# Kernel optimization log

Measured on AMD Instinct MI355X. Metric: run time of the kernel, lower is better.

## Reference

```python
import jax, jax.numpy as jnp
import numpy as np

BS = 16
CIN = 32          # input_channels
COUT = 64         # out_channels
OUT_DIM = 1024    # out_dim
S = 2
S0 = 1
K = S * (S0 + 1)  # non-overlapping patch size = 4
D = OUT_DIM * K   # input spatial length = 4096


def setup_inputs() -> dict:
    key = jax.random.key(0)
    k1, k2 = jax.random.split(key)
    x = jax.random.normal(k1, (BS, CIN, D), dtype=jnp.float32)
    # learned parameter, torch.randn init
    weight = jax.random.normal(k2, (COUT, CIN, D), dtype=jnp.float32)
    return {"x": x, "weight": weight}


def reference(x, weight):
    # sharing == 0 path of NonOverlappingLocallyConnected1d:
    #   out[b,o,p] = (1/sqrt(CIN)) * sum_{c,k} x[b,c,p*K+k] * weight[o,c,p*K+k]
    # Original materializes [bs,cout,cin,D] via broadcast multiply then sums
    # over (cin, K); fused here as a single einsum over non-overlapping patches.
    bs = x.shape[0]
    xr = x.reshape(bs, CIN, OUT_DIM, K)        # [b, c, p, k]
    wr = weight.reshape(COUT, CIN, OUT_DIM, K)  # [o, c, p, k]
    out = jnp.einsum('bcpk,ocpk->bop', xr, wr)  # [b, o, p]
    return out / jnp.sqrt(jnp.asarray(CIN, x.dtype))
```

## Files before the change

### kernel.cpp

```cpp
#include <hip/hip_runtime.h>

#define CIN     32
#define COUT    64
#define OUT_DIM 1024
#define RS4     1024

__global__ __launch_bounds__(512, 2) void nolc1d_kernel(
    const float* __restrict__ x,
    const float* __restrict__ w,
    float* __restrict__ out)
{
    const int bid = blockIdx.x;
    const int xcd = bid & 7;
    const int m   = bid >> 3;
    const int og  = m & 3;
    const int pc  = xcd * 8 + (m >> 2);
    const int o0  = og * 16;
    const int pf0 = pc * 16;

    const int t    = threadIdx.x;
    const int lane = t & 63;
    const int wv   = t >> 6;
    const int p    = t & 15;
    const int cs   = (t >> 4) & 1;
    const int g    = (t >> 5) & 3;
    const int oq   = t >> 7;

    __shared__ float4 wls[3][1024];
    __shared__ float4 xls[3][1024];

    const float4* __restrict__ x4 = (const float4*)x;
    const float4* __restrict__ w4 = (const float4*)w;

    const int r4 = lane >> 4;
    const int q  = lane & 15;

    auto stage = [&](int buf, int ci) {
        #pragma unroll
        for (int i = 0; i < 2; ++i) {
            const int s = wv * 2 + i;
            const int c = ci * 4 + r4;
            const float4* srcw =
                &w4[((o0 + s) * CIN + c) * RS4 + pf0 + q];
            __builtin_amdgcn_global_load_lds(
                (const __attribute__((address_space(1))) void*)srcw,
                (__attribute__((address_space(3))) void*)&wls[buf][s * 64],
                16, 0, 0);
            const float4* srcx =
                &x4[(s * CIN + c) * RS4 + pf0 + q];
            __builtin_amdgcn_global_load_lds(
                (const __attribute__((address_space(1))) void*)srcx,
                (__attribute__((address_space(3))) void*)&xls[buf][s * 64],
                16, 0, 0);
        }
    };

    float acc[4][4] = {};

    stage(0, 0);
    stage(1, 1);

    #pragma unroll 1
    for (int ci = 0; ci < 8; ++ci) {
        if (ci < 7) asm volatile("s_waitcnt vmcnt(4)" ::: "memory");
        else        asm volatile("s_waitcnt vmcnt(0)" ::: "memory");
        __builtin_amdgcn_s_barrier();
        if (ci < 6) stage((ci + 2) % 3, ci + 2);
        const int buf = ci % 3;
        #pragma unroll
        for (int jj = 0; jj < 2; ++jj) {
            const int cl = cs * 2 + jj;
            float4 xv[4], wq[4];
            #pragma unroll
            for (int bi = 0; bi < 4; ++bi)
                xv[bi] = xls[buf][((g * 4 + bi) * 4 + cl) * 16 + p];
            #pragma unroll
            for (int oi = 0; oi < 4; ++oi)
                wq[oi] = wls[buf][((oq * 4 + oi) * 4 + cl) * 16 + p];
            #pragma unroll
            for (int bi = 0; bi < 4; ++bi)
                #pragma unroll
                for (int oi = 0; oi < 4; ++oi)
                    acc[bi][oi] += xv[bi].x * wq[oi].x + xv[bi].y * wq[oi].y +
                                   xv[bi].z * wq[oi].z + xv[bi].w * wq[oi].w;
        }
    }

    #pragma unroll
    for (int bi = 0; bi < 4; ++bi)
        #pragma unroll
        for (int oi = 0; oi < 4; ++oi)
            acc[bi][oi] += __shfl_xor(acc[bi][oi], 16, 64);

    const float scale = 0.17677669529663687f;
    if (cs == 0) {
        #pragma unroll
        for (int bi = 0; bi < 4; ++bi)
            #pragma unroll
            for (int oi = 0; oi < 4; ++oi)
                out[((size_t)(4 * g + bi) * COUT + o0 + 4 * oq + oi) * OUT_DIM
                    + pf0 + p] = acc[bi][oi] * scale;
    }
}

extern "C" void kernel_launch(void* const* d_in, const int* in_sizes, int n_in,
                              void* d_out, int out_size, void* d_ws, size_t ws_size,
                              hipStream_t stream) {
    const float* x = (const float*)d_in[0];
    const float* w = (const float*)d_in[1];
    float* out = (float*)d_out;

    nolc1d_kernel<<<dim3(256), dim3(512), 0, stream>>>(x, w, out);
}
```

Measured before the change: 85.72 us.

## Warp-specialize producer/consumer waves with LDS flag handshakes and 4-stage buffers

Splits the block into two loader waves (one for weights, one for x) and four compute waves, synchronized through volatile LDS flags and done counters instead of block-wide barriers. Grows the LDS ring from three to four stages and swizzles the x layout with an XOR to reduce bank conflicts. Each compute wave now covers all four channels per chunk, so the cross-lane shuffle reduction is gone. It adds spin-wait polling and relies on vmcnt ordering for LDS-direct loads being visible to other waves, which is fragile. The 128KB LDS per block may also cap occupancy at one block per CU.

```diff
diff --git a/kernel.cpp b/kernel.cpp
--- a/kernel.cpp
+++ b/kernel.cpp
@@ -5,7 +5,7 @@
 #define OUT_DIM 1024
 #define RS4     1024
 
-__global__ __launch_bounds__(512, 2) void nolc1d_kernel(
+__global__ __launch_bounds__(384, 2) void nolc1d_kernel(
     const float* __restrict__ x,
     const float* __restrict__ w,
     float* __restrict__ out)
@@ -21,85 +21,112 @@
     const int t    = threadIdx.x;
     const int lane = t & 63;
     const int wv   = t >> 6;
-    const int p    = t & 15;
-    const int cs   = (t >> 4) & 1;
-    const int g    = (t >> 5) & 3;
-    const int oq   = t >> 7;
 
-    __shared__ float4 wls[3][1024];
-    __shared__ float4 xls[3][1024];
+    __shared__ float4 wls[4][1024];
+    __shared__ float4 xls[4][1024];
+    __shared__ int flag_w[8];
+    __shared__ int flag_x[8];
+    __shared__ int done[8];
+
+    if (t < 8) { flag_w[t] = 0; flag_x[t] = 0; done[t] = 0; }
+    __syncthreads();
+
+    volatile int* vfw = flag_w;
+    volatile int* vfx = flag_x;
+    volatile int* vdn = done;
 
     const float4* __restrict__ x4 = (const float4*)x;
     const float4* __restrict__ w4 = (const float4*)w;
 
-    const int r4 = lane >> 4;
-    const int q  = lane & 15;
+    if (wv == 0) {
+        const int cl = lane >> 4;
+        const int q  = lane & 15;
+        #pragma unroll 1
+        for (int ci = 0; ci < 8; ++ci) {
+            if (ci >= 4) while (vdn[ci - 4] < 4) __builtin_amdgcn_s_sleep(1);
+            const int buf = ci & 3;
+            #pragma unroll
+            for (int s = 0; s < 16; ++s) {
+                const float4* src =
+                    &w4[((o0 + s) * CIN + ci * 4 + cl) * RS4 + pf0 + q];
+                __builtin_amdgcn_global_load_lds(
+                    (const __attribute__((address_space(1))) void*)src,
+                    (__attribute__((address_space(3))) void*)&wls[buf][s * 64],
+                    16, 0, 0);
+            }
+            if (ci >= 2) {
+                asm volatile("s_waitcnt vmcnt(32)" ::: "memory");
+                vfw[ci - 2] = 1;
+            }
+        }
+        asm volatile("s_waitcnt vmcnt(16)" ::: "memory");
+        vfw[6] = 1;
+        asm volatile("s_waitcnt vmcnt(0)" ::: "memory");
+        vfw[7] = 1;
+    } else if (wv == 1) {
+        const int cl = lane >> 4;
+        #pragma unroll 1
+        for (int ci = 0; ci < 8; ++ci) {
+            if (ci >= 4) while (vdn[ci - 4] < 4) __builtin_amdgcn_s_sleep(1);
+            const int buf = ci & 3;
+            #pragma unroll
+            for (int s = 0; s < 16; ++s) {
+                const int qs = (lane & 15) ^ (s >> 2);
+                const float4* src =
+                    &x4[(s * CIN + ci * 4 + cl) * RS4 + pf0 + qs];
+                __builtin_amdgcn_global_load_lds(
+                    (const __attribute__((address_space(1))) void*)src,
+                    (__attribute__((address_space(3))) void*)&xls[buf][s * 64],
+                    16, 0, 0);
+            }
+            if (ci >= 2) {
+                asm volatile("s_waitcnt vmcnt(32)" ::: "memory");
+                vfx[ci - 2] = 1;
+            }
+        }
+        asm volatile("s_waitcnt vmcnt(16)" ::: "memory");
+        vfx[6] = 1;
+        asm volatile("s_waitcnt vmcnt(0)" ::: "memory");
+        vfx[7] = 1;
+    } else {
+        const int cw = wv - 2;
+        const int q  = lane & 15;
+        const int g  = lane >> 4;
+        float acc[4][4] = {};
 
-    auto stage = [&](int buf, int ci) {
-        #pragma unroll
-        for (int i = 0; i < 2; ++i) {
-            const int s = wv * 2 + i;
-            const int c = ci * 4 + r4;
-            const float4* srcw =
-                &w4[((o0 + s) * CIN + c) * RS4 + pf0 + q];
-            __builtin_amdgcn_global_load_lds(
-                (const __attribute__((address_space(1))) void*)srcw,
-                (__attribute__((address_space(3))) void*)&wls[buf][s * 64],
-                16, 0, 0);
-            const float4* srcx =
-                &x4[(s * CIN + c) * RS4 + pf0 + q];
-            __builtin_amdgcn_global_load_lds(
-                (const __attribute__((address_space(1))) void*)srcx,
-                (__attribute__((address_space(3))) void*)&xls[buf][s * 64],
-                16, 0, 0);
-        }
-    };
-
-    float acc[4][4] = {};
-
-    stage(0, 0);
-    stage(1, 1);
-
-    #pragma unroll 1
-    for (int ci = 0; ci < 8; ++ci) {
-        if (ci < 7) asm volatile("s_waitcnt vmcnt(4)" ::: "memory");
-        else        asm volatile("s_waitcnt vmcnt(0)" ::: "memory");
-        __builtin_amdgcn_s_barrier();
-        if (ci < 6) stage((ci + 2) % 3, ci + 2);
-        const int buf = ci % 3;
-        #pragma unroll
-        for (int jj = 0; jj < 2; ++jj) {
-            const int cl = cs * 2 + jj;
-            float4 xv[4], wq[4];
+        #pragma unroll 1
+        for (int ci = 0; ci < 8; ++ci) {
+            while (vfw[ci] == 0) __builtin_amdgcn_s_sleep(1);
+            while (vfx[ci] == 0) __builtin_amdgcn_s_sleep(1);
+            const int buf = ci & 3;
             #pragma unroll
-            for (int bi = 0; bi < 4; ++bi)
-                xv[bi] = xls[buf][((g * 4 + bi) * 4 + cl) * 16 + p];
-            #pragma unroll
-            for (int oi = 0; oi < 4; ++oi)
-                wq[oi] = wls[buf][((oq * 4 + oi) * 4 + cl) * 16 + p];
-            #pragma unroll
-            for (int bi = 0; bi < 4; ++bi)
+            for (int cl = 0; cl < 4; ++cl) {
+                float4 xv[4], wq[4];
+                #pragma unroll
+                for (int bi = 0; bi < 4; ++bi)
+                    xv[bi] = xls[buf][((g * 4 + bi) * 4 + cl) * 16 + (q ^ g)];
                 #pragma unroll
                 for (int oi = 0; oi < 4; ++oi)
-                    acc[bi][oi] += xv[bi].x * wq[oi].x + xv[bi].y * wq[oi].y +
-                                   xv[bi].z * wq[oi].z + xv[bi].w * wq[oi].w;
+                    wq[oi] = wls[buf][((cw * 4 + oi) * 4 + cl) * 16 + q];
+                #pragma unroll
+                for (int bi = 0; bi < 4; ++bi)
+                    #pragma unroll
+                    for (int oi = 0; oi < 4; ++oi)
+                        acc[bi][oi] += xv[bi].x * wq[oi].x +
+                                       xv[bi].y * wq[oi].y +
+                                       xv[bi].z * wq[oi].z +
+                                       xv[bi].w * wq[oi].w;
+            }
+            if (lane == 0) atomicAdd(&done[ci], 1);
         }
-    }
 
-    #pragma unroll
-    for (int bi = 0; bi < 4; ++bi)
-        #pragma unroll
-        for (int oi = 0; oi < 4; ++oi)
-            acc[bi][oi] += __shfl_xor(acc[bi][oi], 16, 64);
-
-    const float scale = 0.17677669529663687f;
-    if (cs == 0) {
+        const float scale = 0.17677669529663687f;
         #pragma unroll
         for (int bi = 0; bi < 4; ++bi)
             #pragma unroll
             for (int oi = 0; oi < 4; ++oi)
-                out[((size_t)(4 * g + bi) * COUT + o0 + 4 * oq + oi) * OUT_DIM
-                    + pf0 + p] = acc[bi][oi] * scale;
+                out[((size_t)(4 * g + bi) * COUT + o0 + 4 * cw + oi) * OUT_DIM
+                    + pf0 + q] = acc[bi][oi] * scale;
     }
 }
 
@@ -110,5 +137,5 @@
     const float* w = (const float*)d_in[1];
     float* out = (float*)d_out;
 
-    nolc1d_kernel<<<dim3(256), dim3(512), 0, stream>>>(x, w, out);
+    nolc1d_kernel<<<dim3(256), dim3(384), 0, stream>>>(x, w, out);
 }
```

Result: faster. 83.59 us (-2.5%).
